# Kernel optimization log

Hardware: AMD Instinct MI355X
Metric: run time of the kernel (lower is better)

## Reference

```python
import jax, jax.numpy as jnp
import numpy as np
import math

B, H, W, K, E, FF, L, NH = 16, 64, 64, 2, 512, 2048, 4, 8


def setup_inputs() -> dict:
    key = jax.random.key(0)
    ks = jax.random.split(key, 24)
    s = 0.02
    inp = {
        "data": jax.random.normal(ks[0], (B, H, W), jnp.float32),
        "conv_w": jax.random.normal(ks[1], (K, K), jnp.float32) * 0.5,
        "conv_b": jax.random.normal(ks[2], (), jnp.float32) * 0.1,
        "lin_w": jax.random.normal(ks[3], (E, 1), jnp.float32) * 0.5,
        "lin_b": jax.random.normal(ks[4], (E,), jnp.float32) * 0.1,
        "Wq": jax.random.normal(ks[5], (L, E, E), jnp.float32) * s,
        "bq": jnp.zeros((L, E), jnp.float32),
        "Wk": jax.random.normal(ks[6], (L, E, E), jnp.float32) * s,
        "bk": jnp.zeros((L, E), jnp.float32),
        "Wv": jax.random.normal(ks[7], (L, E, E), jnp.float32) * s,
        "bv": jnp.zeros((L, E), jnp.float32),
        "Wo": jax.random.normal(ks[8], (L, E, E), jnp.float32) * s,
        "bo": jnp.zeros((L, E), jnp.float32),
        "ln1_g": jnp.ones((L, E), jnp.float32),
        "ln1_b": jnp.zeros((L, E), jnp.float32),
        "ln2_g": jnp.ones((L, E), jnp.float32),
        "ln2_b": jnp.zeros((L, E), jnp.float32),
        "W1": jax.random.normal(ks[9], (L, FF, E), jnp.float32) * s,
        "b1": jnp.zeros((L, FF), jnp.float32),
        "W2": jax.random.normal(ks[10], (L, E, FF), jnp.float32) * s,
        "b2": jnp.zeros((L, E), jnp.float32),
        "Wc": jax.random.normal(ks[11], (1, E), jnp.float32) * s,
        "bc": jnp.zeros((1,), jnp.float32),
        "num_heads": NH,
    }
    return inp


def _pos_encoding(seq_len, embed_dim):
    pos = jnp.arange(seq_len, dtype=jnp.float32)[:, None]
    div = jnp.exp(jnp.arange(0, embed_dim, 2, dtype=jnp.float32) * (-math.log(10000.0) / embed_dim))
    pe = jnp.zeros((seq_len, embed_dim), jnp.float32)
    pe = pe.at[:, 0::2].set(jnp.sin(pos * div))
    pe = pe.at[:, 1::2].set(jnp.cos(pos * div))
    return pe


def _layer_norm(x, g, b, eps=1e-5):
    mu = jnp.mean(x, axis=-1, keepdims=True)
    var = jnp.mean(jnp.square(x - mu), axis=-1, keepdims=True)
    return (x - mu) * jax.lax.rsqrt(var + eps) * g + b


def reference(data, conv_w, conv_b, lin_w, lin_b, Wq, bq, Wk, bk, Wv, bv, Wo, bo,
              ln1_g, ln1_b, ln2_g, ln2_b, W1, b1, W2, b2, Wc, bc, num_heads):
    b, h, w = data.shape
    k = conv_w.shape[0]
    # patch extraction == torch unfold(1,k,k).unfold(2,k,k) -> [B, P, k, k]
    patches = data.reshape(b, h // k, k, w // k, k).transpose(0, 1, 3, 2, 4)
    patches = patches.reshape(b, -1, k, k)
    # per-patch conv (k x k kernel on k x k patch -> scalar) + bias
    conv = jnp.einsum('bpij,ij->bp', patches, conv_w) + conv_b  # [B, P]
    # Linear(1 -> E)
    x = conv[..., None] * lin_w[:, 0] + lin_b  # [B, P, E]
    P, e = x.shape[1], x.shape[2]
    x = x + _pos_encoding(P, e)

    dk = e // num_heads
    scale = 1.0 / math.sqrt(dk)
    n_layers = Wq.shape[0]
    for l in range(n_layers):
        q = (x @ Wq[l].T + bq[l]).reshape(b, P, num_heads, dk).transpose(0, 2, 1, 3)
        kk = (x @ Wk[l].T + bk[l]).reshape(b, P, num_heads, dk).transpose(0, 2, 1, 3)
        v = (x @ Wv[l].T + bv[l]).reshape(b, P, num_heads, dk).transpose(0, 2, 1, 3)
        scores = jnp.einsum('bhqd,bhkd->bhqk', q, kk) * scale
        attn = jax.nn.softmax(scores, axis=-1)
        out = jnp.einsum('bhqk,bhkd->bhqd', attn, v)
        out = out.transpose(0, 2, 1, 3).reshape(b, P, e)
        out = out @ Wo[l].T + bo[l]
        x = _layer_norm(x + out, ln1_g[l], ln1_b[l])
        ffn = jax.nn.relu(x @ W1[l].T + b1[l]) @ W2[l].T + b2[l]
        x = _layer_norm(x + ffn, ln2_g[l], ln2_b[l])

    pooled = jnp.mean(x, axis=1)  # [B, E]
    return pooled @ Wc.T + bc  # [B, 1]
```

## Files before the change

### kernel.cpp

```cpp
#include <hip/hip_runtime.h>
#include <math.h>

#define P_SEQ 1024
#define E_DIM 512
#define NHEAD 8
#define DK    64
#define BATCH 16
#define M_TOK (BATCH * P_SEQ)
#define FF_DIM 2048
#define NLAYER 4

#define QSCALE 0.1803368801111204f

typedef __attribute__((ext_vector_type(8))) __bf16 bf16x8;
typedef __attribute__((ext_vector_type(8))) unsigned short ushortx8;
typedef __attribute__((ext_vector_type(4))) float floatx4;
typedef unsigned int u32;
typedef const __attribute__((address_space(1))) u32* gptr_t;
typedef __attribute__((address_space(3))) u32* lptr_t;

__device__ inline float bf2f(unsigned short u) {
  union { unsigned int i; float f; } c; c.i = ((unsigned int)u) << 16; return c.f;
}
__device__ inline unsigned short f2bf(float f) {
  union { float f; unsigned int i; } c; c.f = f;
  unsigned int i = c.i;
  i += 0x7FFFu + ((i >> 16) & 1u);
  return (unsigned short)(i >> 16);
}
__device__ inline bf16x8 ld8(const unsigned short* p) {
  return *reinterpret_cast<const bf16x8*>(p);
}

__global__ void detect_dtype(const unsigned short* __restrict__ data, int* __restrict__ flag) {
  if (threadIdx.x == 0) {
    int sane = 0;
    for (int i = 0; i < 256; i++) {
      int e = (data[i] >> 7) & 0xFF;
      if (e >= 107 && e <= 133) sane++;
    }
    *flag = (sane >= 240) ? 0 : 1;
  }
}

#define C_DATA 0
#define C_WO   65536
#define C_BO   1114112
#define C_LN1G 1116160
#define C_LN1B 1118208
#define C_LN2G 1120256
#define C_LN2B 1122304
#define C_W1   1124352
#define C_B1   5318656
#define C_W2   5326848
#define C_B2   9521152
#define C_CW   9523200
#define C_CB   9523208
#define C_LW   9523216
#define C_LB   9523728
#define C_WC   9524240
#define C_BC   9524752

struct ConvArgs {
  const void* src[23];
  unsigned short* canon;
  unsigned short* wqkv;
  unsigned short* bqkv;
  const int* flag;
};

__global__ __launch_bounds__(256) void convert_pack(ConvArgs a)
{
  const int i = blockIdx.x * 256 + threadIdx.x;
  const bool f32 = (*a.flag != 0);
  #define LOADF(IDX, J) (f32 ? ((const float*)a.src[IDX])[J] \
                             : bf2f(((const unsigned short*)a.src[IDX])[J]))
  int base = 0;
  if (i < base + 1048576) {
    const int j = i - base, l = j >> 18, rem = j & 262143;
    a.wqkv[l * 786432 + rem] = f2bf(LOADF(5, j) * QSCALE);
    return;
  } base += 1048576;
  if (i < base + 1048576) {
    const int j = i - base, l = j >> 18, rem = j & 262143;
    a.wqkv[l * 786432 + 262144 + rem] = f2bf(LOADF(7, j));
    return;
  } base += 1048576;
  if (i < base + 1048576) {
    const int j = i - base, l = j >> 18, rem = j & 262143;
    a.wqkv[l * 786432 + 524288 + rem] = f2bf(LOADF(9, j));
    return;
  } base += 1048576;
  if (i < base + 4194304) {
    const int j = i - base;
    a.canon[C_W1 + j] = f2bf(LOADF(17, j));
    return;
  } base += 4194304;
  if (i < base + 4194304) {
    const int j = i - base;
    a.canon[C_W2 + j] = f2bf(LOADF(19, j));
    return;
  } base += 4194304;
  if (i < base + 1048576) {
    const int j = i - base;
    a.canon[C_WO + j] = f2bf(LOADF(11, j));
    return;
  } base += 1048576;
  if (i < base + 65536) {
    const int j = i - base;
    a.canon[C_DATA + j] = f2bf(LOADF(0, j));
    return;
  } base += 65536;
  if (i < base + 2048) {
    const int j = i - base, l = j >> 9, r = j & 511;
    a.bqkv[l * 1536 + r] = f2bf(LOADF(6, j) * QSCALE);
    return;
  } base += 2048;
  if (i < base + 2048) {
    const int j = i - base, l = j >> 9, r = j & 511;
    a.bqkv[l * 1536 + 512 + r] = f2bf(LOADF(8, j));
    return;
  } base += 2048;
  if (i < base + 2048) {
    const int j = i - base, l = j >> 9, r = j & 511;
    a.bqkv[l * 1536 + 1024 + r] = f2bf(LOADF(10, j));
    return;
  } base += 2048;
  if (i < base + 2048) { a.canon[C_BO   + i - base] = f2bf(LOADF(12, i - base)); return; } base += 2048;
  if (i < base + 2048) { a.canon[C_LN1G + i - base] = f2bf(LOADF(13, i - base)); return; } base += 2048;
  if (i < base + 2048) { a.canon[C_LN1B + i - base] = f2bf(LOADF(14, i - base)); return; } base += 2048;
  if (i < base + 2048) { a.canon[C_LN2G + i - base] = f2bf(LOADF(15, i - base)); return; } base += 2048;
  if (i < base + 2048) { a.canon[C_LN2B + i - base] = f2bf(LOADF(16, i - base)); return; } base += 2048;
  if (i < base + 8192) { a.canon[C_B1   + i - base] = f2bf(LOADF(18, i - base)); return; } base += 8192;
  if (i < base + 2048) { a.canon[C_B2   + i - base] = f2bf(LOADF(20, i - base)); return; } base += 2048;
  if (i < base + 4)   { a.canon[C_CW + i - base] = f2bf(LOADF(1, i - base)); return; } base += 4;
  if (i < base + 1)   { a.canon[C_CB + i - base] = f2bf(LOADF(2, i - base)); return; } base += 1;
  if (i < base + 512) { a.canon[C_LW + i - base] = f2bf(LOADF(3, i - base)); return; } base += 512;
  if (i < base + 512) { a.canon[C_LB + i - base] = f2bf(LOADF(4, i - base)); return; } base += 512;
  if (i < base + 512) { a.canon[C_WC + i - base] = f2bf(LOADF(21, i - base)); return; } base += 512;
  if (i < base + 1)   { a.canon[C_BC + i - base] = f2bf(LOADF(22, i - base)); return; }
  #undef LOADF
}
#define CONV_TOTAL (3*1048576 + 2*4194304 + 1048576 + 65536 + 3*2048 + 7*2048 + 8192 - 2048 + 4 + 1 + 512 + 512 + 512 + 1)

#define BM 128
#define BN 128
#define BK 64

template <int MODE>
__global__ __launch_bounds__(256) void gemm_tile(
    const unsigned short* __restrict__ X, const unsigned short* __restrict__ W,
    const unsigned short* __restrict__ bias, unsigned short* __restrict__ Y,
    int M, int N, int Kd)
{
  __shared__ __align__(16) unsigned short As[2][BM * BK];
  __shared__ __align__(16) unsigned short Bs[2][BN * BK];

  const int tid  = threadIdx.x;
  const int lane = tid & 63;
  const int wave = tid >> 6;
  const int wm = wave & 1, wn = wave >> 1;
  const int col = lane & 15, quad = lane >> 4;

  const int m0 = blockIdx.y * BM;
  const int n0 = blockIdx.x * BN;

  const int srow = tid >> 3;
  const int scb  = tid & 7;

  floatx4 acc[4][4] = {};

  auto stage = [&](int kt, int buf) {
    #pragma unroll
    for (int i = 0; i < 4; i++) {
      const int r  = i * 32 + srow;
      const int cb = scb ^ (r & 7);
      const unsigned short* ga = X + (size_t)(m0 + r) * Kd + kt + cb * 8;
      __builtin_amdgcn_global_load_lds((gptr_t)(const void*)ga,
          (lptr_t)(void*)&As[buf][r * BK + scb * 8], 16, 0, 0);
    }
    #pragma unroll
    for (int i = 0; i < 4; i++) {
      const int r  = i * 32 + srow;
      const int cb = scb ^ (r & 7);
      const unsigned short* gb = W + (size_t)(n0 + r) * Kd + kt + cb * 8;
      __builtin_amdgcn_global_load_lds((gptr_t)(const void*)gb,
          (lptr_t)(void*)&Bs[buf][r * BK + scb * 8], 16, 0, 0);
    }
  };

  const int NT = Kd / BK;
  stage(0, 0);

  for (int c = 0; c < NT; c++) {
    const int buf = c & 1;
    __syncthreads();
    if (c + 1 < NT) stage((c + 1) * BK, buf ^ 1);

    #pragma unroll
    for (int kk = 0; kk < 2; kk++) {
      bf16x8 af[4], bfr[4];
      #pragma unroll
      for (int t = 0; t < 4; t++) {
        const int mr = wm * 64 + t * 16 + col;
        const int ka = (kk * 4 + quad) ^ (mr & 7);
        af[t] = ld8(&As[buf][mr * BK + ka * 8]);
        const int nr = wn * 64 + t * 16 + col;
        const int kb = (kk * 4 + quad) ^ (nr & 7);
        bfr[t] = ld8(&Bs[buf][nr * BK + kb * 8]);
      }
      #pragma unroll
      for (int mt = 0; mt < 4; mt++)
        #pragma unroll
        for (int nt = 0; nt < 4; nt++)
          acc[mt][nt] = __builtin_amdgcn_mfma_f32_16x16x32_bf16(af[mt], bfr[nt], acc[mt][nt], 0, 0, 0);
    }
  }

  #pragma unroll
  for (int nt = 0; nt < 4; nt++) {
    const int c = n0 + wn * 64 + nt * 16 + col;
    const float bb = bf2f(bias[c]);
    #pragma unroll
    for (int mt = 0; mt < 4; mt++) {
      #pragma unroll
      for (int r = 0; r < 4; r++) {
        float v = acc[mt][nt][r] + bb;
        if (MODE == 1) v = fmaxf(v, 0.f);
        const int rr = m0 + wm * 64 + mt * 16 + quad * 4 + r;
        size_t idx;
        if (MODE == 4) {
          const int third = c >> 9, cc = c & 511;
          const int b = rr >> 10, p = rr & 1023;
          const int h = cc >> 6, d = cc & 63;
          if (third < 2)
            idx = (size_t)third * 8388608 + (((size_t)(b * NHEAD + h) * P_SEQ) + p) * DK + d;
          else
            idx = 16777216 + (((size_t)(b * NHEAD + h) * DK) + d) * P_SEQ + p;
        } else {
          idx = (size_t)rr * N + c;
        }
        Y[idx] = f2bf(v);
      }
    }
  }
}

__global__ __launch_bounds__(256, 3) void attn_flash8(
    const unsigned short* __restrict__ Q, const unsigned short* __restrict__ K,
    const unsigned short* __restrict__ Vt, unsigned short* __restrict__ O)
{
  __shared__ __align__(16) unsigned short Ks[2][64 * 64];
  __shared__ __align__(16) unsigned short Vs[2][64 * 64];
  __shared__ __align__(16) unsigned short Ps[4][2][16 * 64];

  const int tid  = threadIdx.x;
  const int lane = tid & 63;
  const int wave = tid >> 6;
  const int col  = lane & 15, quad = lane >> 4;
  const int bh = blockIdx.x & 127;
  const int qb0 = (blockIdx.x >> 7) * 128 + wave * 32;

  const unsigned short* Qh = Q  + (size_t)bh * P_SEQ * DK;
  const unsigned short* Kh = K  + (size_t)bh * P_SEQ * DK;
  const unsigned short* Vh = Vt + (size_t)bh * DK * P_SEQ;

  bf16x8 aq[2][2];
  #pragma unroll
  for (int t = 0; t < 2; t++) {
    aq[t][0] = ld8(Qh + (size_t)(qb0 + t * 16 + col) * DK + quad * 8);
    aq[t][1] = ld8(Qh + (size_t)(qb0 + t * 16 + col) * DK + 32 + quad * 8);
  }

  const ushortx8 one_raw = {0x3F80, 0x3F80, 0x3F80, 0x3F80, 0x3F80, 0x3F80, 0x3F80, 0x3F80};
  const bf16x8 ones = __builtin_bit_cast(bf16x8, one_raw);

  floatx4 o[2][4] = {};
  floatx4 lacc[2] = {};

  const int srow = tid >> 3;
  const int scb  = tid & 7;

  auto stage = [&](int kk, int buf) {
    #pragma unroll
    for (int i = 0; i < 2; i++) {
      const int r  = i * 32 + srow;
      const int cb = scb ^ (r & 7);
      __builtin_amdgcn_global_load_lds(
          (gptr_t)(const void*)(Kh + (size_t)(kk + r) * DK + cb * 8),
          (lptr_t)(void*)&Ks[buf][r * 64 + scb * 8], 16, 0, 0);
      __builtin_amdgcn_global_load_lds(
          (gptr_t)(const void*)(Vh + (size_t)r * P_SEQ + kk + cb * 8),
          (lptr_t)(void*)&Vs[buf][r * 64 + scb * 8], 16, 0, 0);
    }
  };

  stage(0, 0);

  for (int c = 0; c < 16; c++) {
    const int buf = c & 1;
    __syncthreads();
    if (c < 15) stage((c + 1) * 64, buf ^ 1);

    bf16x8 kb0[4], kb1[4];
    #pragma unroll
    for (int nt = 0; nt < 4; nt++) {
      const int kr = nt * 16 + col;
      kb0[nt] = ld8(&Ks[buf][kr * 64 + ((quad       ^ (kr & 7)) << 3)]);
      kb1[nt] = ld8(&Ks[buf][kr * 64 + (((4 + quad) ^ (kr & 7)) << 3)]);
    }

    floatx4 s[2][4] = {};
    #pragma unroll
    for (int t = 0; t < 2; t++)
      #pragma unroll
      for (int nt = 0; nt < 4; nt++) {
        s[t][nt] = __builtin_amdgcn_mfma_f32_16x16x32_bf16(aq[t][0], kb0[nt], s[t][nt], 0, 0, 0);
        s[t][nt] = __builtin_amdgcn_mfma_f32_16x16x32_bf16(aq[t][1], kb1[nt], s[t][nt], 0, 0, 0);
      }

    #pragma unroll
    for (int t = 0; t < 2; t++) {
      #pragma unroll
      for (int r = 0; r < 4; r++) {
        const int row = quad * 4 + r;
        unsigned short* pr = &Ps[wave][t][row * 64];
        #pragma unroll
        for (int nt = 0; nt < 4; nt++) {
          const float p = exp2f(fminf(s[t][nt][r], 126.f));
          union { float f; unsigned int u; } pu; pu.f = p;
          const int key = nt * 16 + col;
          pr[(((key >> 3) ^ (row & 7)) << 3) | (key & 7)] = (unsigned short)(pu.u >> 16);
        }
      }
    }
    __asm__ volatile("s_waitcnt lgkmcnt(0)" ::: "memory");

    bf16x8 pa[2][2];
    #pragma unroll
    for (int t = 0; t < 2; t++) {
      pa[t][0] = ld8(&Ps[wave][t][col * 64 + ((quad       ^ (col & 7)) << 3)]);
      pa[t][1] = ld8(&Ps[wave][t][col * 64 + (((4 + quad) ^ (col & 7)) << 3)]);
    }

    #pragma unroll
    for (int dt = 0; dt < 4; dt++) {
      const int dr = dt * 16 + col;
      const bf16x8 v0 = ld8(&Vs[buf][dr * 64 + ((quad       ^ (dr & 7)) << 3)]);
      const bf16x8 v1 = ld8(&Vs[buf][dr * 64 + (((4 + quad) ^ (dr & 7)) << 3)]);
      #pragma unroll
      for (int t = 0; t < 2; t++) {
        o[t][dt] = __builtin_amdgcn_mfma_f32_16x16x32_bf16(pa[t][0], v0, o[t][dt], 0, 0, 0);
        o[t][dt] = __builtin_amdgcn_mfma_f32_16x16x32_bf16(pa[t][1], v1, o[t][dt], 0, 0, 0);
      }
    }
    #pragma unroll
    for (int t = 0; t < 2; t++) {
      lacc[t] = __builtin_amdgcn_mfma_f32_16x16x32_bf16(pa[t][0], ones, lacc[t], 0, 0, 0);
      lacc[t] = __builtin_amdgcn_mfma_f32_16x16x32_bf16(pa[t][1], ones, lacc[t], 0, 0, 0);
    }
  }

  const int b = bh >> 3, h = bh & 7;
  #pragma unroll
  for (int t = 0; t < 2; t++)
    #pragma unroll
    for (int r = 0; r < 4; r++) {
      const int p = qb0 + t * 16 + quad * 4 + r;
      const float inv = 1.f / lacc[t][r];
      const size_t base = ((size_t)(b * P_SEQ + p)) * E_DIM + h * DK;
      #pragma unroll
      for (int dt = 0; dt < 4; dt++)
        O[base + dt * 16 + col] = f2bf(o[t][dt][r] * inv);
    }
}

__global__ __launch_bounds__(256) void add_ln4(
    unsigned short* __restrict__ X, const unsigned short* __restrict__ R,
    const unsigned short* __restrict__ g, const unsigned short* __restrict__ bta)
{
  const int row  = blockIdx.x * 4 + (threadIdx.x >> 6);
  const int lane = threadIdx.x & 63;
  const size_t base = (size_t)row * E_DIM + lane * 8;

  uint4 xu = *reinterpret_cast<const uint4*>(X + base);
  uint4 ru = *reinterpret_cast<const uint4*>(R + base);
  unsigned int xs[4] = {xu.x, xu.y, xu.z, xu.w};
  unsigned int rs[4] = {ru.x, ru.y, ru.z, ru.w};

  float v[8];
  float s = 0.f;
  #pragma unroll
  for (int i = 0; i < 4; i++) {
    v[2*i]   = bf2f((unsigned short)(xs[i] & 0xffffu)) + bf2f((unsigned short)(rs[i] & 0xffffu));
    v[2*i+1] = bf2f((unsigned short)(xs[i] >> 16))     + bf2f((unsigned short)(rs[i] >> 16));
    s += v[2*i] + v[2*i+1];
  }
  #pragma unroll
  for (int off = 1; off < 64; off <<= 1) s += __shfl_xor(s, off, 64);
  const float mu = s * (1.f / 512.f);

  float var = 0.f;
  #pragma unroll
  for (int i = 0; i < 8; i++) { float d = v[i] - mu; var += d * d; }
  #pragma unroll
  for (int off = 1; off < 64; off <<= 1) var += __shfl_xor(var, off, 64);
  const float rstd = rsqrtf(var * (1.f / 512.f) + 1e-5f);

  unsigned int ow[4];
  #pragma unroll
  for (int i = 0; i < 4; i++) {
    int e0 = lane * 8 + 2 * i;
    float y0 = (v[2*i]   - mu) * rstd * bf2f(g[e0])     + bf2f(bta[e0]);
    float y1 = (v[2*i+1] - mu) * rstd * bf2f(g[e0 + 1]) + bf2f(bta[e0 + 1]);
    ow[i] = (unsigned int)f2bf(y0) | ((unsigned int)f2bf(y1) << 16);
  }
  *reinterpret_cast<uint4*>(X + base) = make_uint4(ow[0], ow[1], ow[2], ow[3]);
}

__global__ __launch_bounds__(64) void embed_kernel(
    const unsigned short* __restrict__ canon, unsigned short* __restrict__ X)
{
  const unsigned short* data   = canon + C_DATA;
  const unsigned short* conv_w = canon + C_CW;
  const unsigned short* conv_b = canon + C_CB;
  const unsigned short* lin_w  = canon + C_LW;
  const unsigned short* lin_b  = canon + C_LB;
  const int bp = blockIdx.x;
  const int b = bp >> 10, p = bp & 1023;
  const int ph = p >> 5, pw = p & 31;
  const unsigned short* dr = data + ((size_t)b * 64 + ph * 2) * 64 + pw * 2;
  const float c = bf2f(dr[0])  * bf2f(conv_w[0]) + bf2f(dr[1])  * bf2f(conv_w[1])
                + bf2f(dr[64]) * bf2f(conv_w[2]) + bf2f(dr[65]) * bf2f(conv_w[3])
                + bf2f(conv_b[0]);
  const int lane = threadIdx.x;
  unsigned int ow[4];
  #pragma unroll
  for (int i = 0; i < 4; i++) {
    const int e0 = lane * 8 + 2 * i;
    const float fr = __expf(-(float)e0 * (9.210340371976184f / 512.f));
    const float ang = (float)p * fr;
    const float v0 = c * bf2f(lin_w[e0])     + bf2f(lin_b[e0])     + sinf(ang);
    const float v1 = c * bf2f(lin_w[e0 + 1]) + bf2f(lin_b[e0 + 1]) + cosf(ang);
    ow[i] = (unsigned int)f2bf(v0) | ((unsigned int)f2bf(v1) << 16);
  }
  *reinterpret_cast<uint4*>(X + (size_t)bp * E_DIM + lane * 8) =
      make_uint4(ow[0], ow[1], ow[2], ow[3]);
}

__global__ __launch_bounds__(256) void classify_partial(
    const unsigned short* __restrict__ X, const unsigned short* __restrict__ Wc,
    float* __restrict__ partial)
{
  const int b = blockIdx.x, sl = blockIdx.y;
  const int tid = threadIdx.x;
  const unsigned short* xb = X + (size_t)b * P_SEQ * E_DIM + (size_t)sl * 128 * E_DIM;
  float s0 = 0.f, s1 = 0.f;
  for (int p = 0; p < 128; p++) {
    s0 += bf2f(xb[(size_t)p * E_DIM + tid]);
    s1 += bf2f(xb[(size_t)p * E_DIM + tid + 256]);
  }
  float acc = s0 * bf2f(Wc[tid]) + s1 * bf2f(Wc[tid + 256]);
  #pragma unroll
  for (int off = 1; off < 64; off <<= 1) acc += __shfl_xor(acc, off, 64);
  __shared__ float red[4];
  if ((tid & 63) == 0) red[tid >> 6] = acc;
  __syncthreads();
  if (tid == 0) partial[b * 8 + sl] = red[0] + red[1] + red[2] + red[3];
}

__global__ __launch_bounds__(64) void classify_final(
    const float* __restrict__ partial, const unsigned short* __restrict__ bc,
    void* __restrict__ out, const int* __restrict__ flag)
{
  const int b = threadIdx.x;
  if (b >= BATCH) return;
  float s = 0.f;
  #pragma unroll
  for (int i = 0; i < 8; i++) s += partial[b * 8 + i];
  float r = s * (1.f / 1024.f) + bf2f(bc[0]);
  if (*flag) ((float*)out)[b] = r;
  else       ((unsigned short*)out)[b] = f2bf(r);
}

extern "C" void kernel_launch(void* const* d_in, const int* in_sizes, int n_in,
                              void* d_out, int out_size, void* d_ws, size_t ws_size,
                              hipStream_t stream)
{
  char* ws = (char*)d_ws;
  const size_t MB = (size_t)1 << 20;

  unsigned short* canon = (unsigned short*)ws;
  int* flag = (int*)(ws + 176 * MB);
  float* partial = (float*)(ws + 176 * MB + 256);
  unsigned short* wqkv = (unsigned short*)(ws + 177 * MB);
  unsigned short* bqkv = (unsigned short*)(ws + 184 * MB);

  unsigned short* x    = (unsigned short*)(ws + 32 * MB);
  unsigned short* qb   = (unsigned short*)(ws + 48 * MB);
  unsigned short* attn = (unsigned short*)(ws + 96 * MB);
  unsigned short* hbuf = (unsigned short*)(ws + 112 * MB);
  unsigned short* obuf = (unsigned short*)(ws + 144 * MB);
  unsigned short* fbuf = attn;

  const unsigned short* kb  = qb + 8388608;
  const unsigned short* vtb = qb + 16777216;

  detect_dtype<<<1, 64, 0, stream>>>((const unsigned short*)d_in[0], flag);

  ConvArgs ca;
  for (int i = 0; i < 23; i++) ca.src[i] = d_in[i];
  ca.canon = canon; ca.wqkv = wqkv; ca.bqkv = bqkv; ca.flag = flag;
  convert_pack<<<(CONV_TOTAL + 255) / 256, 256, 0, stream>>>(ca);

  embed_kernel<<<dim3(M_TOK), dim3(64), 0, stream>>>(canon, x);

  for (int l = 0; l < NLAYER; l++) {
    const unsigned short* Wqkv_l = wqkv + (size_t)l * 1536 * 512;
    const unsigned short* bqkv_l = bqkv + l * 1536;
    const unsigned short* Wo_l = canon + C_WO + (size_t)l * E_DIM * E_DIM;
    const unsigned short* W1_l = canon + C_W1 + (size_t)l * FF_DIM * E_DIM;
    const unsigned short* W2_l = canon + C_W2 + (size_t)l * E_DIM * FF_DIM;

    gemm_tile<4><<<dim3(1536 / BN, M_TOK / BM), dim3(256), 0, stream>>>(
        x, Wqkv_l, bqkv_l, qb, M_TOK, 1536, E_DIM);

    attn_flash8<<<dim3((P_SEQ / 128) * BATCH * NHEAD), dim3(256), 0, stream>>>(
        qb, kb, vtb, attn);

    gemm_tile<0><<<dim3(E_DIM / BN, M_TOK / BM), dim3(256), 0, stream>>>(
        attn, Wo_l, canon + C_BO + l * E_DIM, obuf, M_TOK, E_DIM, E_DIM);
    add_ln4<<<dim3(M_TOK / 4), dim3(256), 0, stream>>>(
        x, obuf, canon + C_LN1G + l * E_DIM, canon + C_LN1B + l * E_DIM);

    gemm_tile<1><<<dim3(FF_DIM / BN, M_TOK / BM), dim3(256), 0, stream>>>(
        x, W1_l, canon + C_B1 + l * FF_DIM, hbuf, M_TOK, FF_DIM, E_DIM);
    gemm_tile<0><<<dim3(E_DIM / BN, M_TOK / BM), dim3(256), 0, stream>>>(
        hbuf, W2_l, canon + C_B2 + l * E_DIM, fbuf, M_TOK, E_DIM, FF_DIM);
    add_ln4<<<dim3(M_TOK / 4), dim3(256), 0, stream>>>(
        x, fbuf, canon + C_LN2G + l * E_DIM, canon + C_LN2B + l * E_DIM);
  }

  classify_partial<<<dim3(BATCH, 8), dim3(256), 0, stream>>>(x, canon + C_WC, partial);
  classify_final<<<dim3(1), dim3(64), 0, stream>>>(partial, canon + C_BC, d_out, flag);
}
```

Before: 1.181 ms.

## Remap GEMM B-tile columns so each lane owns four adjacent outputs for vector stores

Changes the B-fragment row mapping in the GEMM so each lane's four N-tiles are consecutive columns, with an adjusted LDS swizzle to match. The epilogue can then write four packed bf16 values per store (uint2) instead of scalar 16-bit stores, including a dedicated path for the transposed V output in the QKV mode. It also adds a packed hardware bf16 conversion helper, used in the GEMM epilogue, layernorm and embedding. The aim is to cut epilogue store instructions and conversion ALU work, at the risk of new LDS bank conflicts from the changed swizzle.

```diff
diff --git a/kernel.cpp b/kernel.cpp
--- a/kernel.cpp
+++ b/kernel.cpp
@@ -13,7 +13,6 @@
 #define QSCALE 0.1803368801111204f
 
 typedef __attribute__((ext_vector_type(8))) __bf16 bf16x8;
-typedef __attribute__((ext_vector_type(8))) unsigned short ushortx8;
 typedef __attribute__((ext_vector_type(4))) float floatx4;
 typedef unsigned int u32;
 typedef const __attribute__((address_space(1))) u32* gptr_t;
@@ -30,6 +29,16 @@
 }
 __device__ inline bf16x8 ld8(const unsigned short* p) {
   return *reinterpret_cast<const bf16x8*>(p);
+}
+
+__device__ inline unsigned int pkbf16(float lo, float hi) {
+#if defined(__HIP_DEVICE_COMPILE__) && __has_builtin(__builtin_amdgcn_cvt_pk_bf16_f32)
+  typedef __attribute__((ext_vector_type(2))) __bf16 bf16x2;
+  bf16x2 v = __builtin_amdgcn_cvt_pk_bf16_f32(lo, hi);
+  return __builtin_bit_cast(unsigned int, v);
+#else
+  return (unsigned int)f2bf(lo) | ((unsigned int)f2bf(hi) << 16);
+#endif
 }
 
 __global__ void detect_dtype(const unsigned short* __restrict__ data, int* __restrict__ flag) {
@@ -182,7 +191,7 @@
     #pragma unroll
     for (int i = 0; i < 4; i++) {
       const int r  = i * 32 + srow;
-      const int cb = scb ^ (r & 7);
+      const int cb = scb ^ ((r >> 2) & 7);
       const unsigned short* gb = W + (size_t)(n0 + r) * Kd + kt + cb * 8;
       __builtin_amdgcn_global_load_lds((gptr_t)(const void*)gb,
           (lptr_t)(void*)&Bs[buf][r * BK + scb * 8], 16, 0, 0);
@@ -205,8 +214,8 @@
         const int mr = wm * 64 + t * 16 + col;
         const int ka = (kk * 4 + quad) ^ (mr & 7);
         af[t] = ld8(&As[buf][mr * BK + ka * 8]);
-        const int nr = wn * 64 + t * 16 + col;
-        const int kb = (kk * 4 + quad) ^ (nr & 7);
+        const int nr = wn * 64 + col * 4 + t;
+        const int kb = (kk * 4 + quad) ^ (col & 7);
         bfr[t] = ld8(&Bs[buf][nr * BK + kb * 8]);
       }
       #pragma unroll
@@ -217,34 +226,61 @@
     }
   }
 
-  #pragma unroll
-  for (int nt = 0; nt < 4; nt++) {
-    const int c = n0 + wn * 64 + nt * 16 + col;
-    const float bb = bf2f(bias[c]);
+  const int col4 = n0 + wn * 64 + col * 4;
+  float bb[4];
+  {
+    const uint2 bu = *reinterpret_cast<const uint2*>(&bias[col4]);
+    bb[0] = bf2f((unsigned short)(bu.x & 0xffffu));
+    bb[1] = bf2f((unsigned short)(bu.x >> 16));
+    bb[2] = bf2f((unsigned short)(bu.y & 0xffffu));
+    bb[3] = bf2f((unsigned short)(bu.y >> 16));
+  }
+
+  if (MODE == 4 && (col4 >> 9) == 2) {
+    const int cc0 = col4 & 511;
+    const int h = cc0 >> 6;
+    #pragma unroll
+    for (int nt = 0; nt < 4; nt++) {
+      const int d = (cc0 + nt) & 63;
+      #pragma unroll
+      for (int mt = 0; mt < 4; mt++) {
+        const int p0 = m0 + wm * 64 + mt * 16 + quad * 4;
+        const int b = p0 >> 10, p = p0 & 1023;
+        float v0 = acc[mt][nt][0] + bb[nt], v1 = acc[mt][nt][1] + bb[nt];
+        float v2 = acc[mt][nt][2] + bb[nt], v3 = acc[mt][nt][3] + bb[nt];
+        const size_t idx = 16777216 + (((size_t)(b * NHEAD + h) * DK) + d) * P_SEQ + p;
+        *reinterpret_cast<uint2*>(&Y[idx]) = make_uint2(pkbf16(v0, v1), pkbf16(v2, v3));
+      }
+    }
+  } else {
+    const int third = col4 >> 9;
+    const int cc0 = col4 & 511;
+    const int h = cc0 >> 6, d0 = cc0 & 63;
     #pragma unroll
     for (int mt = 0; mt < 4; mt++) {
       #pragma unroll
       for (int r = 0; r < 4; r++) {
-        float v = acc[mt][nt][r] + bb;
-        if (MODE == 1) v = fmaxf(v, 0.f);
         const int rr = m0 + wm * 64 + mt * 16 + quad * 4 + r;
+        float v0 = acc[mt][0][r] + bb[0], v1 = acc[mt][1][r] + bb[1];
+        float v2 = acc[mt][2][r] + bb[2], v3 = acc[mt][3][r] + bb[3];
+        if (MODE == 1) {
+          v0 = fmaxf(v0, 0.f); v1 = fmaxf(v1, 0.f);
+          v2 = fmaxf(v2, 0.f); v3 = fmaxf(v3, 0.f);
+        }
         size_t idx;
         if (MODE == 4) {
-          const int third = c >> 9, cc = c & 511;
           const int b = rr >> 10, p = rr & 1023;
-          const int h = cc >> 6, d = cc & 63;
-          if (third < 2)
-            idx = (size_t)third * 8388608 + (((size_t)(b * NHEAD + h) * P_SEQ) + p) * DK + d;
-          else
-            idx = 16777216 + (((size_t)(b * NHEAD + h) * DK) + d) * P_SEQ + p;
+          idx = (size_t)third * 8388608 + (((size_t)(b * NHEAD + h) * P_SEQ) + p) * DK + d0;
         } else {
-          idx = (size_t)rr * N + c;
+          idx = (size_t)rr * N + col4;
         }
-        Y[idx] = f2bf(v);
+        *reinterpret_cast<uint2*>(&Y[idx]) = make_uint2(pkbf16(v0, v1), pkbf16(v2, v3));
       }
     }
   }
 }
+
+typedef __attribute__((ext_vector_type(8))) unsigned short ushortx8;
 
 __global__ __launch_bounds__(256, 3) void attn_flash8(
     const unsigned short* __restrict__ Q, const unsigned short* __restrict__ K,
@@ -413,7 +449,7 @@
     int e0 = lane * 8 + 2 * i;
     float y0 = (v[2*i]   - mu) * rstd * bf2f(g[e0])     + bf2f(bta[e0]);
     float y1 = (v[2*i+1] - mu) * rstd * bf2f(g[e0 + 1]) + bf2f(bta[e0 + 1]);
-    ow[i] = (unsigned int)f2bf(y0) | ((unsigned int)f2bf(y1) << 16);
+    ow[i] = pkbf16(y0, y1);
   }
   *reinterpret_cast<uint4*>(X + base) = make_uint4(ow[0], ow[1], ow[2], ow[3]);
 }
@@ -442,7 +478,7 @@
     const float ang = (float)p * fr;
     const float v0 = c * bf2f(lin_w[e0])     + bf2f(lin_b[e0])     + sinf(ang);
     const float v1 = c * bf2f(lin_w[e0 + 1]) + bf2f(lin_b[e0 + 1]) + cosf(ang);
-    ow[i] = (unsigned int)f2bf(v0) | ((unsigned int)f2bf(v1) << 16);
+    ow[i] = pkbf16(v0, v1);
   }
   *reinterpret_cast<uint4*>(X + (size_t)bp * E_DIM + lane * 8) =
       make_uint4(ow[0], ow[1], ow[2], ow[3]);
```

Result: faster. 1.099 ms (-6.9%).
